# Kernel tuning notes

Measured on AMD Instinct MI355X. Metric: run time of the kernel, lower is better.

Reference implementation:

```python
import jax, jax.numpy as jnp
import numpy as np


def setup_inputs() -> dict:
    key = jax.random.key(0)
    k1, k2 = jax.random.split(key)
    batch, cw_dim = 4096, 1024
    dim_embedding, book_size = 8, 256
    dim_codes = cw_dim // dim_embedding  # 128
    x = jax.random.normal(k1, (batch, cw_dim), dtype=jnp.float32)
    codebook = jax.random.normal(k2, (dim_codes, book_size, dim_embedding), dtype=jnp.float32)
    return {"x": x, "codebook": codebook}


def reference(x, codebook):
    # Faithful JAX version of VQVAE.quantise:
    #   pairwise squared distance -> argmin -> gather embeddings -> one-hot scatter
    C, K, D = codebook.shape          # dim_codes, book_size, dim_embedding
    B = x.shape[0]
    xr = x.reshape(B, C, D)           # [B, C, D] (= view(batch*dim_codes, 1, D))
    x2 = jnp.sum(xr * xr, axis=-1)                       # [B, C]
    c2 = jnp.sum(codebook * codebook, axis=-1)           # [C, K]
    dist = x2[..., None] - 2.0 * jnp.einsum('bcd,ckd->bck', xr, codebook) + c2[None]
    idx = jnp.argmin(dist, axis=-1)                      # [B, C]
    # gather nearest codebook entry per code slot
    cw_embed = codebook[jnp.arange(C)[None, :], idx]     # [B, C, D]
    cw_embed = cw_embed.reshape(B, C * D)                # [B, cw_dim]
    # one-hot scatter of selected indices
    one_hot_idx = jax.nn.one_hot(idx, K, dtype=jnp.float32)  # [B, C, K]
    return cw_embed, one_hot_idx
```

## Files before the change

kernel.cpp:

```cpp
#include <hip/hip_runtime.h>


constexpr int B_  = 4096;
constexpr int C_  = 128;
constexpr int K_  = 256;
constexpr int D_  = 8;
constexpr int TPB = 256;
constexpr int NP  = B_ * C_;

typedef float vf4 __attribute__((ext_vector_type(4)));

constexpr int   BPT1   = 8;
constexpr int   BTILE1 = TPB * BPT1;
constexpr float TAU2   = 1.0e-3f;

__global__ __launch_bounds__(TPB) void vq_screen_fix(
    const float* __restrict__ x,
    const float* __restrict__ cb,
    int* __restrict__ idx_out)
{
    __shared__ float s_cbf[K_ * D_];
    __shared__ float s_c2f[K_];

    const int c     = blockIdx.x;
    const int btile = blockIdx.y;
    const int tid   = threadIdx.x;
    const int lane  = tid & 63;

    {
        const float4* gcb = (const float4*)(cb + (size_t)c * (K_ * D_));
        ((float4*)s_cbf)[tid]       = gcb[tid];
        ((float4*)s_cbf)[tid + TPB] = gcb[tid + TPB];
    }
    __syncthreads();
    {
        const float* v = s_cbf + tid * D_;
        float s = 0.f;
        #pragma unroll
        for (int d = 0; d < D_; ++d) s = fmaf(v[d], v[d], s);
        s_c2f[tid] = s;
    }
    __syncthreads();

    float xf[BPT1][D_];
    #pragma unroll
    for (int j = 0; j < BPT1; ++j) {
        const int b = btile * BTILE1 + j * TPB + tid;
        const float4* xp = (const float4*)(x + (size_t)b * (C_ * D_) + c * D_);
        const float4 a = xp[0];
        const float4 h = xp[1];
        xf[j][0] = a.x; xf[j][1] = a.y; xf[j][2] = a.z; xf[j][3] = a.w;
        xf[j][4] = h.x; xf[j][5] = h.y; xf[j][6] = h.z; xf[j][7] = h.w;
    }

    float s1[BPT1], s2[BPT1];
    int   k1[BPT1];
    #pragma unroll
    for (int j = 0; j < BPT1; ++j) { s1[j] = 3.4e38f; s2[j] = 3.4e38f; k1[j] = 0; }

    const float4* scb4 = (const float4*)s_cbf;
    #pragma unroll 2
    for (int k = 0; k < K_; ++k) {
        const float4 clo = scb4[k * 2];
        const float4 chi = scb4[k * 2 + 1];
        const float  c2k = s_c2f[k];
        #pragma unroll
        for (int j = 0; j < BPT1; ++j) {
            float dot = xf[j][0] * clo.x;
            dot = fmaf(xf[j][1], clo.y, dot);
            dot = fmaf(xf[j][2], clo.z, dot);
            dot = fmaf(xf[j][3], clo.w, dot);
            dot = fmaf(xf[j][4], chi.x, dot);
            dot = fmaf(xf[j][5], chi.y, dot);
            dot = fmaf(xf[j][6], chi.z, dot);
            dot = fmaf(xf[j][7], chi.w, dot);
            const float score = fmaf(-2.f, dot, c2k);
            s2[j] = fminf(s2[j], fmaxf(score, s1[j]));
            const bool lt = score < s1[j];
            k1[j] = lt ? k : k1[j];
            s1[j] = lt ? score : s1[j];
        }
    }

    #pragma unroll
    for (int j = 0; j < BPT1; ++j) {
        const bool amb = (s2[j] - s1[j]) <= TAU2;
        unsigned long long mask = __ballot(amb);
        while (mask) {
            const int src = (int)__ffsll((long long)mask) - 1;
            mask &= mask - 1;
            double xd[D_];
            #pragma unroll
            for (int d = 0; d < D_; ++d) xd[d] = (double)__shfl(xf[j][d], src);
            double best = 1.0e300;
            int    bk   = 0;
            #pragma unroll
            for (int t = 0; t < 4; ++t) {
                const int k = lane * 4 + t;
                const float* cv = s_cbf + k * D_;
                double cd[D_];
                #pragma unroll
                for (int d = 0; d < D_; ++d) cd[d] = (double)cv[d];
                double c2k = 0.0;
                #pragma unroll
                for (int d = 0; d < D_; ++d) c2k = fma(cd[d], cd[d], c2k);
                double dot = xd[0] * cd[0];
                #pragma unroll
                for (int d = 1; d < D_; ++d) dot = fma(xd[d], cd[d], dot);
                const double score = fma(-2.0, dot, c2k);
                if (score < best) { best = score; bk = k; }
            }
            #pragma unroll
            for (int off = 32; off >= 1; off >>= 1) {
                const double ob  = __shfl_down(best, off);
                const int    obk = __shfl_down(bk,   off);
                if (ob < best) { best = ob; bk = obk; }
            }
            const int win = __shfl(bk, 0);
            if (lane == src) k1[j] = win;
        }
    }

    #pragma unroll
    for (int j = 0; j < BPT1; ++j) {
        const int b = btile * BTILE1 + j * TPB + tid;
        idx_out[(size_t)b * C_ + c] = k1[j];
    }
}

constexpr int GRID3 = 2048;
constexpr int RPB   = NP / GRID3;

__global__ __launch_bounds__(TPB, 4) void vq_write(
    const int*   __restrict__ idx,
    const float* __restrict__ cb,
    float* __restrict__ out_embed,
    float* __restrict__ out_onehot)
{
    const int tid  = threadIdx.x;
    const int lane = tid & 63;
    const int wave = tid >> 6;
    const int blk  = blockIdx.x;

    const int rowbase = blk * RPB + wave * 64;
    const int myk = idx[rowbase + lane];
    const int e0 = lane * 4;
    #pragma unroll 4
    for (int i = 0; i < 64; ++i) {
        const int k = __builtin_amdgcn_readlane(myk, i);
        vf4 v;
        v.x = (k == e0    ) ? 1.f : 0.f;
        v.y = (k == e0 + 1) ? 1.f : 0.f;
        v.z = (k == e0 + 2) ? 1.f : 0.f;
        v.w = (k == e0 + 3) ? 1.f : 0.f;
        vf4* dst = (vf4*)(out_onehot + (size_t)(rowbase + i) * K_) + lane;
        __builtin_nontemporal_store(v, dst);
    }

    const size_t pbase = (size_t)blk * RPB;
    #pragma unroll
    for (int i = 0; i < 2; ++i) {
        const int    f    = i * TPB + tid;
        const int    pl   = f >> 1;
        const int    half = f & 1;
        const size_t pair = pbase + pl;
        const int    c    = (int)(pair & (C_ - 1));
        const int    k    = idx[pair];
        const vf4 val = ((const vf4*)(cb + ((size_t)c * K_ + k) * D_))[half];
        __builtin_nontemporal_store(val, (vf4*)(out_embed + pbase * D_) + f);
    }
}

extern "C" void kernel_launch(void* const* d_in, const int* in_sizes, int n_in,
                              void* d_out, int out_size, void* d_ws, size_t ws_size,
                              hipStream_t stream) {
    const float* x  = (const float*)d_in[0];
    const float* cb = (const float*)d_in[1];
    float* out        = (float*)d_out;
    float* out_embed  = out;
    float* out_onehot = out + (size_t)B_ * C_ * D_;
    int*   idx_ws     = (int*)d_ws;

    dim3 grid1(C_, B_ / BTILE1);
    vq_screen_fix<<<grid1, TPB, 0, stream>>>(x, cb, idx_ws);

    vq_write<<<GRID3, TPB, 0, stream>>>(idx_ws, cb, out_embed, out_onehot);
}
```

Before: 602.2 us.

## Fuse argmin screening with one-hot and embedding writes into one kernel

Merges the distance/argmin kernel and the output-writing kernel into a single kernel. Each block now processes its batch tile in two passes with fewer rows per thread, then writes embeddings from the shared-memory codebook and one-hot rows directly. This removes the index workspace round trip and a second launch. The trade-off is strided embedding and one-hot store patterns per code slot and a smaller grid.

```diff
diff --git a/kernel.cpp b/kernel.cpp
--- a/kernel.cpp
+++ b/kernel.cpp
@@ -6,26 +6,28 @@
 constexpr int K_  = 256;
 constexpr int D_  = 8;
 constexpr int TPB = 256;
-constexpr int NP  = B_ * C_;
+
+constexpr int   BPT    = 2;
+constexpr int   PASSES = 2;
+constexpr int   BTILE  = TPB * BPT * PASSES;
+constexpr float TAU2   = 1.0e-3f;
 
 typedef float vf4 __attribute__((ext_vector_type(4)));
 
-constexpr int   BPT1   = 8;
-constexpr int   BTILE1 = TPB * BPT1;
-constexpr float TAU2   = 1.0e-3f;
-
-__global__ __launch_bounds__(TPB) void vq_screen_fix(
+__global__ __launch_bounds__(TPB) void vq_fused(
     const float* __restrict__ x,
     const float* __restrict__ cb,
-    int* __restrict__ idx_out)
+    float* __restrict__ out_embed,
+    float* __restrict__ out_onehot)
 {
     __shared__ float s_cbf[K_ * D_];
     __shared__ float s_c2f[K_];
 
-    const int c     = blockIdx.x;
-    const int btile = blockIdx.y;
-    const int tid   = threadIdx.x;
-    const int lane  = tid & 63;
+    const int c    = blockIdx.x;
+    const int bt   = blockIdx.y;
+    const int tid  = threadIdx.x;
+    const int lane = tid & 63;
+    const int wave = tid >> 6;
 
     {
         const float4* gcb = (const float4*)(cb + (size_t)c * (K_ * D_));
@@ -42,132 +44,112 @@
     }
     __syncthreads();
 
-    float xf[BPT1][D_];
-    #pragma unroll
-    for (int j = 0; j < BPT1; ++j) {
-        const int b = btile * BTILE1 + j * TPB + tid;
-        const float4* xp = (const float4*)(x + (size_t)b * (C_ * D_) + c * D_);
-        const float4 a = xp[0];
-        const float4 h = xp[1];
-        xf[j][0] = a.x; xf[j][1] = a.y; xf[j][2] = a.z; xf[j][3] = a.w;
-        xf[j][4] = h.x; xf[j][5] = h.y; xf[j][6] = h.z; xf[j][7] = h.w;
-    }
+    const float4* scb4 = (const float4*)s_cbf;
 
-    float s1[BPT1], s2[BPT1];
-    int   k1[BPT1];
-    #pragma unroll
-    for (int j = 0; j < BPT1; ++j) { s1[j] = 3.4e38f; s2[j] = 3.4e38f; k1[j] = 0; }
+    for (int pass = 0; pass < PASSES; ++pass) {
+        const int bbase = bt * BTILE + pass * (TPB * BPT);
 
-    const float4* scb4 = (const float4*)s_cbf;
-    #pragma unroll 2
-    for (int k = 0; k < K_; ++k) {
-        const float4 clo = scb4[k * 2];
-        const float4 chi = scb4[k * 2 + 1];
-        const float  c2k = s_c2f[k];
+        float xf[BPT][D_];
         #pragma unroll
-        for (int j = 0; j < BPT1; ++j) {
-            float dot = xf[j][0] * clo.x;
-            dot = fmaf(xf[j][1], clo.y, dot);
-            dot = fmaf(xf[j][2], clo.z, dot);
-            dot = fmaf(xf[j][3], clo.w, dot);
-            dot = fmaf(xf[j][4], chi.x, dot);
-            dot = fmaf(xf[j][5], chi.y, dot);
-            dot = fmaf(xf[j][6], chi.z, dot);
-            dot = fmaf(xf[j][7], chi.w, dot);
-            const float score = fmaf(-2.f, dot, c2k);
-            s2[j] = fminf(s2[j], fmaxf(score, s1[j]));
-            const bool lt = score < s1[j];
-            k1[j] = lt ? k : k1[j];
-            s1[j] = lt ? score : s1[j];
+        for (int j = 0; j < BPT; ++j) {
+            const int b = bbase + j * TPB + tid;
+            const float4* xp = (const float4*)(x + (size_t)b * (C_ * D_) + c * D_);
+            const float4 a = xp[0];
+            const float4 h = xp[1];
+            xf[j][0] = a.x; xf[j][1] = a.y; xf[j][2] = a.z; xf[j][3] = a.w;
+            xf[j][4] = h.x; xf[j][5] = h.y; xf[j][6] = h.z; xf[j][7] = h.w;
         }
-    }
 
-    #pragma unroll
-    for (int j = 0; j < BPT1; ++j) {
-        const bool amb = (s2[j] - s1[j]) <= TAU2;
-        unsigned long long mask = __ballot(amb);
-        while (mask) {
-            const int src = (int)__ffsll((long long)mask) - 1;
-            mask &= mask - 1;
-            double xd[D_];
+        float s1[BPT], s2[BPT];
+        int   k1[BPT];
+        #pragma unroll
+        for (int j = 0; j < BPT; ++j) { s1[j] = 3.4e38f; s2[j] = 3.4e38f; k1[j] = 0; }
+
+        #pragma unroll 2
+        for (int k = 0; k < K_; ++k) {
+            const float4 clo = scb4[k * 2];
+            const float4 chi = scb4[k * 2 + 1];
+            const float  c2k = s_c2f[k];
             #pragma unroll
-            for (int d = 0; d < D_; ++d) xd[d] = (double)__shfl(xf[j][d], src);
-            double best = 1.0e300;
-            int    bk   = 0;
-            #pragma unroll
-            for (int t = 0; t < 4; ++t) {
-                const int k = lane * 4 + t;
-                const float* cv = s_cbf + k * D_;
-                double cd[D_];
+            for (int j = 0; j < BPT; ++j) {
+                float dot = xf[j][0] * clo.x;
+                dot = fmaf(xf[j][1], clo.y, dot);
+                dot = fmaf(xf[j][2], clo.z, dot);
+                dot = fmaf(xf[j][3], clo.w, dot);
+                dot = fmaf(xf[j][4], chi.x, dot);
+                dot = fmaf(xf[j][5], chi.y, dot);
+                dot = fmaf(xf[j][6], chi.z, dot);
+                dot = fmaf(xf[j][7], chi.w, dot);
+                const float score = fmaf(-2.f, dot, c2k);
+                s2[j] = fminf(s2[j], fmaxf(score, s1[j]));
+                const bool lt = score < s1[j];
+                k1[j] = lt ? k : k1[j];
+                s1[j] = lt ? score : s1[j];
+            }
+        }
+
+        #pragma unroll
+        for (int j = 0; j < BPT; ++j) {
+            const bool amb = (s2[j] - s1[j]) <= TAU2;
+            unsigned long long mask = __ballot(amb);
+            while (mask) {
+                const int src = (int)__ffsll((long long)mask) - 1;
+                mask &= mask - 1;
+                double xd[D_];
                 #pragma unroll
-                for (int d = 0; d < D_; ++d) cd[d] = (double)cv[d];
-                double c2k = 0.0;
+                for (int d = 0; d < D_; ++d) xd[d] = (double)__shfl(xf[j][d], src);
+                double best = 1.0e300;
+                int    bk   = 0;
                 #pragma unroll
-                for (int d = 0; d < D_; ++d) c2k = fma(cd[d], cd[d], c2k);
-                double dot = xd[0] * cd[0];
+                for (int t = 0; t < 4; ++t) {
+                    const int k = lane * 4 + t;
+                    const float* cv = s_cbf + k * D_;
+                    double cd[D_];
+                    #pragma unroll
+                    for (int d = 0; d < D_; ++d) cd[d] = (double)cv[d];
+                    double c2k = 0.0;
+                    #pragma unroll
+                    for (int d = 0; d < D_; ++d) c2k = fma(cd[d], cd[d], c2k);
+                    double dot = xd[0] * cd[0];
+                    #pragma unroll
+                    for (int d = 1; d < D_; ++d) dot = fma(xd[d], cd[d], dot);
+                    const double score = fma(-2.0, dot, c2k);
+                    if (score < best) { best = score; bk = k; }
+                }
                 #pragma unroll
-                for (int d = 1; d < D_; ++d) dot = fma(xd[d], cd[d], dot);
-                const double score = fma(-2.0, dot, c2k);
-                if (score < best) { best = score; bk = k; }
+                for (int off = 32; off >= 1; off >>= 1) {
+                    const double ob  = __shfl_down(best, off);
+                    const int    obk = __shfl_down(bk,   off);
+                    if (ob < best) { best = ob; bk = obk; }
+                }
+                const int win = __shfl(bk, 0);
+                if (lane == src) k1[j] = win;
             }
-            #pragma unroll
-            for (int off = 32; off >= 1; off >>= 1) {
-                const double ob  = __shfl_down(best, off);
-                const int    obk = __shfl_down(bk,   off);
-                if (ob < best) { best = ob; bk = obk; }
+        }
+
+        #pragma unroll
+        for (int j = 0; j < BPT; ++j) {
+            const int    b    = bbase + j * TPB + tid;
+            const size_t pair = (size_t)b * C_ + c;
+            float4* dst = (float4*)(out_embed + pair * D_);
+            dst[0] = ((const float4*)s_cbf)[k1[j] * 2];
+            dst[1] = ((const float4*)s_cbf)[k1[j] * 2 + 1];
+
+            const int bw = bbase + j * TPB + wave * 64;
+            const int e0 = lane * 4;
+            #pragma unroll 8
+            for (int i = 0; i < 64; ++i) {
+                const int k = __builtin_amdgcn_readlane(k1[j], i);
+                vf4 v;
+                v.x = (k == e0    ) ? 1.f : 0.f;
+                v.y = (k == e0 + 1) ? 1.f : 0.f;
+                v.z = (k == e0 + 2) ? 1.f : 0.f;
+                v.w = (k == e0 + 3) ? 1.f : 0.f;
+                const size_t row = (size_t)(bw + i) * C_ + c;
+                vf4* oh = (vf4*)(out_onehot + row * K_) + lane;
+                __builtin_nontemporal_store(v, oh);
             }
-            const int win = __shfl(bk, 0);
-            if (lane == src) k1[j] = win;
         }
-    }
-
-    #pragma unroll
-    for (int j = 0; j < BPT1; ++j) {
-        const int b = btile * BTILE1 + j * TPB + tid;
-        idx_out[(size_t)b * C_ + c] = k1[j];
-    }
-}
-
-constexpr int GRID3 = 2048;
-constexpr int RPB   = NP / GRID3;
-
-__global__ __launch_bounds__(TPB, 4) void vq_write(
-    const int*   __restrict__ idx,
-    const float* __restrict__ cb,
-    float* __restrict__ out_embed,
-    float* __restrict__ out_onehot)
-{
-    const int tid  = threadIdx.x;
-    const int lane = tid & 63;
-    const int wave = tid >> 6;
-    const int blk  = blockIdx.x;
-
-    const int rowbase = blk * RPB + wave * 64;
-    const int myk = idx[rowbase + lane];
-    const int e0 = lane * 4;
-    #pragma unroll 4
-    for (int i = 0; i < 64; ++i) {
-        const int k = __builtin_amdgcn_readlane(myk, i);
-        vf4 v;
-        v.x = (k == e0    ) ? 1.f : 0.f;
-        v.y = (k == e0 + 1) ? 1.f : 0.f;
-        v.z = (k == e0 + 2) ? 1.f : 0.f;
-        v.w = (k == e0 + 3) ? 1.f : 0.f;
-        vf4* dst = (vf4*)(out_onehot + (size_t)(rowbase + i) * K_) + lane;
-        __builtin_nontemporal_store(v, dst);
-    }
-
-    const size_t pbase = (size_t)blk * RPB;
-    #pragma unroll
-    for (int i = 0; i < 2; ++i) {
-        const int    f    = i * TPB + tid;
-        const int    pl   = f >> 1;
-        const int    half = f & 1;
-        const size_t pair = pbase + pl;
-        const int    c    = (int)(pair & (C_ - 1));
-        const int    k    = idx[pair];
-        const vf4 val = ((const vf4*)(cb + ((size_t)c * K_ + k) * D_))[half];
-        __builtin_nontemporal_store(val, (vf4*)(out_embed + pbase * D_) + f);
     }
 }
 
@@ -179,10 +161,7 @@
     float* out        = (float*)d_out;
     float* out_embed  = out;
     float* out_onehot = out + (size_t)B_ * C_ * D_;
-    int*   idx_ws     = (int*)d_ws;
 
-    dim3 grid1(C_, B_ / BTILE1);
-    vq_screen_fix<<<grid1, TPB, 0, stream>>>(x, cb, idx_ws);
-
-    vq_write<<<GRID3, TPB, 0, stream>>>(idx_ws, cb, out_embed, out_onehot);
+    dim3 grid(C_, B_ / BTILE);
+    vq_fused<<<grid, TPB, 0, stream>>>(x, cb, out_embed, out_onehot);
 }
```

Result: no change. 595.0 us (-1.2%).
